# Kernel optimization log

Measured on AMD Instinct MI355X. Metric: run time of the kernel, lower is better.

Reference implementation:

```python
import jax, jax.numpy as jnp
import numpy as np

N, L, H, D = 4, 2048, 16, 32   # batch, seq len, heads, projection_dim
DIM = H * D                     # 512 model dim


def setup_inputs() -> dict:
    rng = jax.random.key(0)
    k1, k2, k3, k4, k5 = jax.random.split(rng, 5)
    query = jax.random.normal(k1, (N, L, DIM), dtype=jnp.float32)
    key = jax.random.normal(k2, (N, L, DIM), dtype=jnp.float32)
    scale = 0.02
    Wq = jax.random.normal(k3, (DIM, DIM), dtype=jnp.float32) * scale
    Wk = jax.random.normal(k4, (DIM, DIM), dtype=jnp.float32) * scale
    Wv = jax.random.normal(k5, (DIM, DIM), dtype=jnp.float32) * scale
    return {"query": query, "key": key, "Wq": Wq, "Wk": Wk, "Wv": Wv, "mask": 1}


def reference(query, key, Wq, Wk, Wv, mask):
    # torch Linear(bias=False): y = x @ W^T
    n, Lq, _ = query.shape
    _, Lk, _ = key.shape
    q = (query @ Wq.T).reshape(n, Lq, H, D).transpose(0, 2, 1, 3)  # (N,H,Lq,D)
    k = (key @ Wk.T).reshape(n, Lk, H, D).transpose(0, 2, 1, 3)    # (N,H,Lk,D)
    v = (key @ Wv.T).reshape(n, Lk, H, D).transpose(0, 2, 1, 3)    # (N,H,Lk,D)
    q = jax.nn.softmax(q, axis=-1)
    k = jax.nn.softmax(k, axis=-1)
    # causal branch (mask truthy): Lq*Lk > D^2*Lk, so the module takes the
    # cumsum-of-outer-products ("right") path:
    #   right = cumsum_l( k_l outer v_l );  out_l = q_l @ right_l
    kv = jnp.einsum('nhld,nhle->nhlde', k, v)   # (N,H,Lk,D,D) outer products
    S = jnp.cumsum(kv, axis=2)                  # running prefix state
    out = jnp.einsum('nhld,nhlde->nhle', q, S)  # (N,H,Lq,D)
    return out.transpose(0, 2, 1, 3).reshape(n, Lq, H * D)
```

## Files before the change

### kernel.cpp

```cpp
#include <hip/hip_runtime.h>

#define NB      4
#define L_SEQ   2048
#define H_HEADS 16
#define D32     32
#define DIM     512
#define NH      (NB * H_HEADS)
#define CHUNK   64
#define NCHUNK  (L_SEQ / CHUNK)

typedef __attribute__((ext_vector_type(8))) short bf16x8;
typedef __attribute__((ext_vector_type(4))) float f32x4;

__device__ __forceinline__ unsigned short f2bf(float x) {
    unsigned u = __float_as_uint(x);
    u += 0x7fff + ((u >> 16) & 1);
    return (unsigned short)(u >> 16);
}
__device__ __forceinline__ unsigned pack2(float lo, float hi) {
    return (unsigned)f2bf(lo) | ((unsigned)f2bf(hi) << 16);
}

#define QN  4194304
#define WN  262144
#define TOT (2*QN + 3*WN)
__global__ __launch_bounds__(256) void convert_kernel(
    const float* __restrict__ query, const float* __restrict__ key,
    const float* __restrict__ Wq, const float* __restrict__ Wk,
    const float* __restrict__ Wv, unsigned short* __restrict__ dst)
{
    int idx = (blockIdx.x * 256 + threadIdx.x) * 8;
    const float* src; int off;
    if (idx < QN)               { src = query; off = idx; }
    else if (idx < 2*QN)        { src = key;   off = idx - QN; }
    else if (idx < 2*QN + WN)   { src = Wq;    off = idx - 2*QN; }
    else if (idx < 2*QN + 2*WN) { src = Wk;    off = idx - 2*QN - WN; }
    else                        { src = Wv;    off = idx - 2*QN - 2*WN; }
    float4 a = *(const float4*)(src + off);
    float4 b = *(const float4*)(src + off + 4);
    *(uint4*)(dst + idx) = make_uint4(pack2(a.x, a.y), pack2(a.z, a.w),
                                      pack2(b.x, b.y), pack2(b.z, b.w));
}

__device__ __forceinline__ void softmax_heads(f32x4 (&acc)[4][4]) {
    #pragma unroll
    for (int i = 0; i < 4; i++)
        #pragma unroll
        for (int jp = 0; jp < 2; jp++)
            #pragma unroll
            for (int r = 0; r < 4; r++) {
                float a = acc[i][2 * jp][r], b = acc[i][2 * jp + 1][r];
                float m = fmaxf(a, b);
                #pragma unroll
                for (int off = 1; off < 16; off <<= 1)
                    m = fmaxf(m, __shfl_xor(m, off, 64));
                float ea = __expf(a - m), eb = __expf(b - m);
                float s = ea + eb;
                #pragma unroll
                for (int off = 1; off < 16; off <<= 1)
                    s += __shfl_xor(s, off, 64);
                float inv = 1.0f / s;
                acc[i][2 * jp][r]     = ea * inv;
                acc[i][2 * jp + 1][r] = eb * inv;
            }
}

__device__ __forceinline__ void scatter_qk(
    const f32x4 (&acc)[4][4], unsigned short* __restrict__ dp,
    int m0, int n0, int wm, int wn, int quad, int lm)
{
    #pragma unroll
    for (int i = 0; i < 4; i++) {
        int rbase = m0 + wm * 64 + i * 16 + quad * 4;
        #pragma unroll
        for (int r = 0; r < 4; r++) {
            int rg = rbase + r;
            int n = rg >> 11, l = rg & 2047;
            #pragma unroll
            for (int j = 0; j < 4; j++) {
                int cg = n0 + wn * 64 + j * 16 + lm;
                int h = cg >> 5, e = cg & 31;
                dp[(((size_t)(n * H_HEADS + h)) * L_SEQ + l) * D32 + e] =
                    f2bf(acc[i][j][r]);
            }
        }
    }
}

#define GLL(g, l) __builtin_amdgcn_global_load_lds( \
    (const __attribute__((address_space(1))) unsigned int*)(g), \
    (__attribute__((address_space(3))) unsigned int*)(l), 16, 0, 0)

__global__ __launch_bounds__(256, 2) void gemm3_mfma_kernel(
    const unsigned short* __restrict__ qb, const unsigned short* __restrict__ kb2,
    const unsigned short* __restrict__ wqb, const unsigned short* __restrict__ wkb,
    const unsigned short* __restrict__ wvb,
    unsigned short* __restrict__ Qs, unsigned short* __restrict__ Ks,
    unsigned short* __restrict__ Vt)
{
    const int z  = blockIdx.z;
    const int bx = blockIdx.x >> 6;
    const int by = blockIdx.x & 63;
    const int m0 = by * 128, n0 = bx * 128;

    const unsigned short* PA  = z ? kb2 : qb;
    const unsigned short* PB1 = z ? wkb : wqb;

    __shared__ unsigned short Asm[3 * 4096];
    __shared__ unsigned short B1sm[3 * 4096];
    __shared__ unsigned short B2sm[3 * 4096];

    const int t    = threadIdx.x;
    const int w    = t >> 6;
    const int lane = t & 63;
    const int wm   = w >> 1, wn = w & 1;
    const int lm   = lane & 15, quad = lane >> 4;

    const int qswz = quad ^ ((lm >> 1) & 3);
    const int aoff = (wm * 64 + lm) * 32 + qswz * 8;
    const int boff = (wn * 64 + lm) * 32 + qswz * 8;

    const int li0 = t, li1 = t + 256;
    const int row0 = li0 >> 2, row1 = li1 >> 2;
    const int qs0 = (li0 & 3) ^ ((li0 >> 3) & 3);
    const int qs1 = (li1 & 3) ^ ((li1 >> 3) & 3);
    const unsigned short* gA0 = PA  + (size_t)(m0 + row0) * DIM + qs0 * 8;
    const unsigned short* gA1 = PA  + (size_t)(m0 + row1) * DIM + qs1 * 8;
    const unsigned short* gB10 = PB1 + (size_t)(n0 + row0) * DIM + qs0 * 8;
    const unsigned short* gB11 = PB1 + (size_t)(n0 + row1) * DIM + qs1 * 8;

    if (z == 0) {
        f32x4 acc[4][4] = {};
#define STG0(buf, kb) do { \
        GLL(gA0  + (kb), Asm  + (buf) * 4096 + li0 * 8); \
        GLL(gB10 + (kb), B1sm + (buf) * 4096 + li0 * 8); \
        GLL(gA1  + (kb), Asm  + (buf) * 4096 + li1 * 8); \
        GLL(gB11 + (kb), B1sm + (buf) * 4096 + li1 * 8); \
} while (0)
        STG0(0, 0);
        STG0(1, 32);
        __builtin_amdgcn_sched_barrier(0);
        asm volatile("s_waitcnt vmcnt(4)" ::: "memory");
        __builtin_amdgcn_s_barrier();
        __builtin_amdgcn_sched_barrier(0);

        #pragma unroll
        for (int step = 0; step < 16; ++step) {
            const int cur = step % 3;
            if (step < 14) STG0((step + 2) % 3, (step + 2) * 32);
            const unsigned short* As = Asm + cur * 4096;
            const unsigned short* Bs = B1sm + cur * 4096;
            bf16x8 af[4], bf1[4];
            #pragma unroll
            for (int i = 0; i < 4; i++)
                af[i] = *(const bf16x8*)(As + aoff + i * 512);
            #pragma unroll
            for (int j = 0; j < 4; j++)
                bf1[j] = *(const bf16x8*)(Bs + boff + j * 512);
            #pragma unroll
            for (int i = 0; i < 4; i++)
                #pragma unroll
                for (int j = 0; j < 4; j++)
                    acc[i][j] = __builtin_amdgcn_mfma_f32_16x16x32_bf16(
                        af[i], bf1[j], acc[i][j], 0, 0, 0);
            __builtin_amdgcn_sched_barrier(0);
            if (step < 14)       asm volatile("s_waitcnt vmcnt(4)" ::: "memory");
            else if (step == 14) asm volatile("s_waitcnt vmcnt(0)" ::: "memory");
            if (step < 15) {
                __builtin_amdgcn_s_barrier();
                __builtin_amdgcn_sched_barrier(0);
            }
        }
#undef STG0
        softmax_heads(acc);
        scatter_qk(acc, Qs, m0, n0, wm, wn, quad, lm);
    } else {
        const unsigned short* gB20 = wvb + (size_t)(n0 + row0) * DIM + qs0 * 8;
        const unsigned short* gB21 = wvb + (size_t)(n0 + row1) * DIM + qs1 * 8;
        f32x4 acc[4][4] = {};
        f32x4 acc2[4][4] = {};
#define STG1(buf, kb) do { \
        GLL(gA0  + (kb), Asm  + (buf) * 4096 + li0 * 8); \
        GLL(gB10 + (kb), B1sm + (buf) * 4096 + li0 * 8); \
        GLL(gB20 + (kb), B2sm + (buf) * 4096 + li0 * 8); \
        GLL(gA1  + (kb), Asm  + (buf) * 4096 + li1 * 8); \
        GLL(gB11 + (kb), B1sm + (buf) * 4096 + li1 * 8); \
        GLL(gB21 + (kb), B2sm + (buf) * 4096 + li1 * 8); \
} while (0)
        STG1(0, 0);
        STG1(1, 32);
        __builtin_amdgcn_sched_barrier(0);
        asm volatile("s_waitcnt vmcnt(6)" ::: "memory");
        __builtin_amdgcn_s_barrier();
        __builtin_amdgcn_sched_barrier(0);

        #pragma unroll
        for (int step = 0; step < 16; ++step) {
            const int cur = step % 3;
            if (step < 14) STG1((step + 2) % 3, (step + 2) * 32);
            const unsigned short* As  = Asm  + cur * 4096;
            const unsigned short* B1s = B1sm + cur * 4096;
            const unsigned short* B2s = B2sm + cur * 4096;
            bf16x8 af[4], bf1[4], bf2[4];
            #pragma unroll
            for (int i = 0; i < 4; i++)
                af[i] = *(const bf16x8*)(As + aoff + i * 512);
            #pragma unroll
            for (int j = 0; j < 4; j++) {
                bf1[j] = *(const bf16x8*)(B1s + boff + j * 512);
                bf2[j] = *(const bf16x8*)(B2s + boff + j * 512);
            }
            #pragma unroll
            for (int i = 0; i < 4; i++)
                #pragma unroll
                for (int j = 0; j < 4; j++) {
                    acc[i][j]  = __builtin_amdgcn_mfma_f32_16x16x32_bf16(
                        af[i], bf1[j], acc[i][j], 0, 0, 0);
                    acc2[i][j] = __builtin_amdgcn_mfma_f32_16x16x32_bf16(
                        af[i], bf2[j], acc2[i][j], 0, 0, 0);
                }
            __builtin_amdgcn_sched_barrier(0);
            if (step < 14)       asm volatile("s_waitcnt vmcnt(6)" ::: "memory");
            else if (step == 14) asm volatile("s_waitcnt vmcnt(0)" ::: "memory");
            if (step < 15) {
                __builtin_amdgcn_s_barrier();
                __builtin_amdgcn_sched_barrier(0);
            }
        }
#undef STG1
        softmax_heads(acc);
        scatter_qk(acc, Ks, m0, n0, wm, wn, quad, lm);
        #pragma unroll
        for (int i = 0; i < 4; i++) {
            int lg0 = m0 + wm * 64 + i * 16 + quad * 4;
            int nb = lg0 >> 11, ll = lg0 & 2047;
            #pragma unroll
            for (int j = 0; j < 4; j++) {
                int cg = n0 + wn * 64 + j * 16 + lm;
                int h = cg >> 5, e = cg & 31;
                ushort4 u;
                u.x = f2bf(acc2[i][j][0]); u.y = f2bf(acc2[i][j][1]);
                u.z = f2bf(acc2[i][j][2]); u.w = f2bf(acc2[i][j][3]);
                *(ushort4*)(Vt + (((size_t)(nb * H_HEADS + h)) * D32 + e) * L_SEQ + ll) = u;
            }
        }
    }
}

__global__ __launch_bounds__(64) void chunk_kv_mfma_kernel(
    const unsigned short* __restrict__ Ks, const unsigned short* __restrict__ Vt,
    float* __restrict__ ckvT)
{
    const int c = blockIdx.x, nh = blockIdx.y;
    const int lane = threadIdx.x;
    const int lm = lane & 15, quad = lane >> 4;

    __shared__ unsigned short Kl[64 * 36];

    {
        const unsigned short* kg = Ks + ((size_t)nh * L_SEQ + c * CHUNK + lane) * D32;
        #pragma unroll
        for (int i = 0; i < 4; i++) {
            uint4 v = *(const uint4*)(kg + i * 8);
            *(uint4*)(Kl + lane * 36 + i * 8) = v;
        }
    }
    __syncthreads();

    f32x4 acc[2][2] = {};
    #pragma unroll
    for (int ch = 0; ch < 2; ch++) {
        bf16x8 aV[2], bK[2];
        #pragma unroll
        for (int mt = 0; mt < 2; mt++)
            aV[mt] = *(const bf16x8*)(Vt + ((size_t)nh * D32 + mt * 16 + lm) * L_SEQ
                                         + c * CHUNK + ch * 32 + quad * 8);
        #pragma unroll
        for (int nt = 0; nt < 2; nt++) {
            const unsigned short* kp = Kl + (ch * 32 + quad * 8) * 36 + nt * 16 + lm;
            #pragma unroll
            for (int j = 0; j < 8; j++) bK[nt][j] = (short)kp[j * 36];
        }
        #pragma unroll
        for (int mt = 0; mt < 2; mt++)
            #pragma unroll
            for (int nt = 0; nt < 2; nt++)
                acc[mt][nt] = __builtin_amdgcn_mfma_f32_16x16x32_bf16(
                    aV[mt], bK[nt], acc[mt][nt], 0, 0, 0);
    }
    #pragma unroll
    for (int mt = 0; mt < 2; mt++)
        #pragma unroll
        for (int nt = 0; nt < 2; nt++)
            #pragma unroll
            for (int r = 0; r < 4; r++) {
                int e = mt * 16 + quad * 4 + r;
                int d = nt * 16 + lm;
                ckvT[(((size_t)nh * NCHUNK + c) * 32 + e) * 32 + d] = acc[mt][nt][r];
            }
}

__global__ __launch_bounds__(64) void prefix_kernel(
    const float* __restrict__ ckvT, unsigned short* __restrict__ SpT)
{
    int nh   = blockIdx.y;
    int slot = blockIdx.x * 64 + threadIdx.x;
    const float* base = ckvT + (size_t)nh * NCHUNK * 1024 + slot * 4;
    unsigned short* sp = SpT + (size_t)nh * NCHUNK * 1024 + slot * 4;
    float4 acc = make_float4(0.f, 0.f, 0.f, 0.f);
    #pragma unroll
    for (int cb = 0; cb < NCHUNK; cb += 8) {
        float4 v[8];
        #pragma unroll
        for (int j = 0; j < 8; j++)
            v[j] = *(const float4*)(base + (size_t)(cb + j) * 1024);
        #pragma unroll
        for (int j = 0; j < 8; j++) {
            ushort4 u;
            u.x = f2bf(acc.x); u.y = f2bf(acc.y);
            u.z = f2bf(acc.z); u.w = f2bf(acc.w);
            *(ushort4*)(sp + (size_t)(cb + j) * 1024) = u;
            acc.x += v[j].x; acc.y += v[j].y;
            acc.z += v[j].z; acc.w += v[j].w;
        }
    }
}

__global__ __launch_bounds__(64) void chunk_out_mfma_kernel(
    const unsigned short* __restrict__ Qs, const unsigned short* __restrict__ Ks,
    const unsigned short* __restrict__ Vt, const unsigned short* __restrict__ SpT,
    float* __restrict__ out)
{
    const int c = blockIdx.x, nh = blockIdx.y;
    __shared__ unsigned short P[64 * 72];

    const int lane = threadIdx.x;
    const int lm = lane & 15, quad = lane >> 4;

    bf16x8 aQ[4], bK[4];
    #pragma unroll
    for (int i = 0; i < 4; i++)
        aQ[i] = *(const bf16x8*)(Qs + ((size_t)nh * L_SEQ + c * CHUNK + i * 16 + lm) * D32
                                    + quad * 8);
    #pragma unroll
    for (int j = 0; j < 4; j++)
        bK[j] = *(const bf16x8*)(Ks + ((size_t)nh * L_SEQ + c * CHUNK + j * 16 + lm) * D32
                                    + quad * 8);

    #pragma unroll
    for (int i = 0; i < 4; i++) {
        #pragma unroll
        for (int j = 0; j < 4; j++) {
            f32x4 p = {};
            if (j <= i) {
                p = __builtin_amdgcn_mfma_f32_16x16x32_bf16(aQ[i], bK[j], p, 0, 0, 0);
                if (j == i) {
                    #pragma unroll
                    for (int r = 0; r < 4; r++)
                        if (lm > quad * 4 + r) p[r] = 0.f;
                }
            }
            #pragma unroll
            for (int r = 0; r < 4; r++)
                P[(i * 16 + quad * 4 + r) * 72 + j * 16 + lm] = f2bf(p[r]);
        }
    }
    __syncthreads();

    bf16x8 bS[2], bV[2][2];
    #pragma unroll
    for (int nt = 0; nt < 2; nt++) {
        bS[nt] = *(const bf16x8*)(SpT + (((size_t)nh * NCHUNK + c) * 32 + nt * 16 + lm) * 32
                                      + quad * 8);
        #pragma unroll
        for (int ch = 0; ch < 2; ch++)
            bV[nt][ch] = *(const bf16x8*)(Vt + ((size_t)nh * D32 + nt * 16 + lm) * L_SEQ
                                             + c * CHUNK + ch * 32 + quad * 8);
    }

    const int n = nh >> 4, h = nh & 15;
    #pragma unroll
    for (int i = 0; i < 4; i++) {
        const int chmax = (i >> 1) + 1;
        bf16x8 aP[2];
        for (int ch = 0; ch < chmax; ch++)
            aP[ch] = *(const bf16x8*)&P[(i * 16 + lm) * 72 + ch * 32 + quad * 8];
        #pragma unroll
        for (int nt = 0; nt < 2; nt++) {
            f32x4 acc = {};
            acc = __builtin_amdgcn_mfma_f32_16x16x32_bf16(aQ[i], bS[nt], acc, 0, 0, 0);
            for (int ch = 0; ch < chmax; ch++)
                acc = __builtin_amdgcn_mfma_f32_16x16x32_bf16(aP[ch], bV[nt][ch], acc, 0, 0, 0);
            #pragma unroll
            for (int r = 0; r < 4; r++) {
                int lg = c * CHUNK + i * 16 + quad * 4 + r;
                out[((size_t)n * L_SEQ + lg) * DIM + h * D32 + nt * 16 + lm] = acc[r];
            }
        }
    }
}

extern "C" void kernel_launch(void* const* d_in, const int* in_sizes, int n_in,
                              void* d_out, int out_size, void* d_ws, size_t ws_size,
                              hipStream_t stream)
{
    (void)in_sizes; (void)n_in; (void)out_size; (void)ws_size;
    const float* query = (const float*)d_in[0];
    const float* key   = (const float*)d_in[1];
    const float* Wq    = (const float*)d_in[2];
    const float* Wk    = (const float*)d_in[3];
    const float* Wv    = (const float*)d_in[4];
    float* out = (float*)d_out;

    unsigned short* bf = (unsigned short*)d_ws;
    unsigned short* qb  = bf;
    unsigned short* kb  = qb + QN;
    unsigned short* wqb = kb + QN;
    unsigned short* wkb = wqb + WN;
    unsigned short* wvb = wkb + WN;
    unsigned short* Qs  = wvb + WN;
    const size_t SZ = (size_t)NH * L_SEQ * D32;
    unsigned short* Ks  = Qs + SZ;
    unsigned short* Vt  = Ks + SZ;
    unsigned short* SpT = Vt + SZ;
    float* ckvT = (float*)(SpT + (size_t)NH * NCHUNK * 1024);

    convert_kernel<<<dim3(TOT / (256 * 8)), dim3(256), 0, stream>>>(
        query, key, Wq, Wk, Wv, qb);
    gemm3_mfma_kernel<<<dim3(256, 1, 2), dim3(256), 0, stream>>>(
        qb, kb, wqb, wkb, wvb, Qs, Ks, Vt);
    chunk_kv_mfma_kernel<<<dim3(NCHUNK, NH), dim3(64), 0, stream>>>(Ks, Vt, ckvT);
    prefix_kernel<<<dim3(4, NH), dim3(64), 0, stream>>>(ckvT, SpT);
    chunk_out_mfma_kernel<<<dim3(NCHUNK, NH), dim3(64), 0, stream>>>(Qs, Ks, Vt, SpT, out);
}
```

Measured before the change: 133.6 us.

## Fuse chunk KV outer products and prefix scan into one per-head kernel

The GEMM epilogue now also writes a transposed K copy (KsT) next to V, so the chunk KV kernel can load K fragments directly instead of going through a strided LDS gather. Chunk KV products and the prefix scan are merged into a single kernel per (batch, head). Each block keeps all 32 chunk states in 128KB of LDS and scans them there, which removes the fp32 ckvT round trip through global memory and one launch. The cost is an extra global write of K, and only 64 blocks of 512 threads with heavy LDS use, so parallelism is much lower.

```diff
diff --git a/kernel.cpp b/kernel.cpp
--- a/kernel.cpp
+++ b/kernel.cpp
@@ -96,7 +96,7 @@
     const unsigned short* __restrict__ wqb, const unsigned short* __restrict__ wkb,
     const unsigned short* __restrict__ wvb,
     unsigned short* __restrict__ Qs, unsigned short* __restrict__ Ks,
-    unsigned short* __restrict__ Vt)
+    unsigned short* __restrict__ Vt, unsigned short* __restrict__ KsT)
 {
     const int z  = blockIdx.z;
     const int bx = blockIdx.x >> 6;
@@ -238,91 +238,71 @@
             for (int j = 0; j < 4; j++) {
                 int cg = n0 + wn * 64 + j * 16 + lm;
                 int h = cg >> 5, e = cg & 31;
-                ushort4 u;
-                u.x = f2bf(acc2[i][j][0]); u.y = f2bf(acc2[i][j][1]);
-                u.z = f2bf(acc2[i][j][2]); u.w = f2bf(acc2[i][j][3]);
-                *(ushort4*)(Vt + (((size_t)(nb * H_HEADS + h)) * D32 + e) * L_SEQ + ll) = u;
-            }
-        }
-    }
-}
-
-__global__ __launch_bounds__(64) void chunk_kv_mfma_kernel(
-    const unsigned short* __restrict__ Ks, const unsigned short* __restrict__ Vt,
-    float* __restrict__ ckvT)
-{
-    const int c = blockIdx.x, nh = blockIdx.y;
-    const int lane = threadIdx.x;
+                size_t base = (((size_t)(nb * H_HEADS + h)) * D32 + e) * L_SEQ + ll;
+                ushort4 uk, uv;
+                uk.x = f2bf(acc[i][j][0]);  uk.y = f2bf(acc[i][j][1]);
+                uk.z = f2bf(acc[i][j][2]);  uk.w = f2bf(acc[i][j][3]);
+                uv.x = f2bf(acc2[i][j][0]); uv.y = f2bf(acc2[i][j][1]);
+                uv.z = f2bf(acc2[i][j][2]); uv.w = f2bf(acc2[i][j][3]);
+                *(ushort4*)(KsT + base) = uk;
+                *(ushort4*)(Vt  + base) = uv;
+            }
+        }
+    }
+}
+
+__global__ __launch_bounds__(512) void kv_prefix_kernel(
+    const unsigned short* __restrict__ KsT, const unsigned short* __restrict__ Vt,
+    unsigned short* __restrict__ SpT)
+{
+    const int nh = blockIdx.x;
+    __shared__ float L[NCHUNK * 1024];
+
+    const int t = threadIdx.x;
+    const int w = t >> 6, lane = t & 63;
     const int lm = lane & 15, quad = lane >> 4;
 
-    __shared__ unsigned short Kl[64 * 36];
-
-    {
-        const unsigned short* kg = Ks + ((size_t)nh * L_SEQ + c * CHUNK + lane) * D32;
-        #pragma unroll
-        for (int i = 0; i < 4; i++) {
-            uint4 v = *(const uint4*)(kg + i * 8);
-            *(uint4*)(Kl + lane * 36 + i * 8) = v;
-        }
+    #pragma unroll
+    for (int cc = 0; cc < 4; cc++) {
+        const int c = w * 4 + cc;
+        f32x4 acc[2][2] = {};
+        #pragma unroll
+        for (int ch = 0; ch < 2; ch++) {
+            bf16x8 aV[2], bK[2];
+            #pragma unroll
+            for (int mt = 0; mt < 2; mt++)
+                aV[mt] = *(const bf16x8*)(Vt + ((size_t)nh * D32 + mt * 16 + lm) * L_SEQ
+                                             + c * CHUNK + ch * 32 + quad * 8);
+            #pragma unroll
+            for (int nt = 0; nt < 2; nt++)
+                bK[nt] = *(const bf16x8*)(KsT + ((size_t)nh * D32 + nt * 16 + lm) * L_SEQ
+                                              + c * CHUNK + ch * 32 + quad * 8);
+            #pragma unroll
+            for (int mt = 0; mt < 2; mt++)
+                #pragma unroll
+                for (int nt = 0; nt < 2; nt++)
+                    acc[mt][nt] = __builtin_amdgcn_mfma_f32_16x16x32_bf16(
+                        aV[mt], bK[nt], acc[mt][nt], 0, 0, 0);
+        }
+        #pragma unroll
+        for (int mt = 0; mt < 2; mt++)
+            #pragma unroll
+            for (int nt = 0; nt < 2; nt++)
+                #pragma unroll
+                for (int r = 0; r < 4; r++)
+                    L[c * 1024 + (mt * 16 + quad * 4 + r) * 32 + nt * 16 + lm]
+                        = acc[mt][nt][r];
     }
     __syncthreads();
 
-    f32x4 acc[2][2] = {};
-    #pragma unroll
-    for (int ch = 0; ch < 2; ch++) {
-        bf16x8 aV[2], bK[2];
-        #pragma unroll
-        for (int mt = 0; mt < 2; mt++)
-            aV[mt] = *(const bf16x8*)(Vt + ((size_t)nh * D32 + mt * 16 + lm) * L_SEQ
-                                         + c * CHUNK + ch * 32 + quad * 8);
-        #pragma unroll
-        for (int nt = 0; nt < 2; nt++) {
-            const unsigned short* kp = Kl + (ch * 32 + quad * 8) * 36 + nt * 16 + lm;
-            #pragma unroll
-            for (int j = 0; j < 8; j++) bK[nt][j] = (short)kp[j * 36];
-        }
-        #pragma unroll
-        for (int mt = 0; mt < 2; mt++)
-            #pragma unroll
-            for (int nt = 0; nt < 2; nt++)
-                acc[mt][nt] = __builtin_amdgcn_mfma_f32_16x16x32_bf16(
-                    aV[mt], bK[nt], acc[mt][nt], 0, 0, 0);
-    }
-    #pragma unroll
-    for (int mt = 0; mt < 2; mt++)
-        #pragma unroll
-        for (int nt = 0; nt < 2; nt++)
-            #pragma unroll
-            for (int r = 0; r < 4; r++) {
-                int e = mt * 16 + quad * 4 + r;
-                int d = nt * 16 + lm;
-                ckvT[(((size_t)nh * NCHUNK + c) * 32 + e) * 32 + d] = acc[mt][nt][r];
-            }
-}
-
-__global__ __launch_bounds__(64) void prefix_kernel(
-    const float* __restrict__ ckvT, unsigned short* __restrict__ SpT)
-{
-    int nh   = blockIdx.y;
-    int slot = blockIdx.x * 64 + threadIdx.x;
-    const float* base = ckvT + (size_t)nh * NCHUNK * 1024 + slot * 4;
-    unsigned short* sp = SpT + (size_t)nh * NCHUNK * 1024 + slot * 4;
-    float4 acc = make_float4(0.f, 0.f, 0.f, 0.f);
-    #pragma unroll
-    for (int cb = 0; cb < NCHUNK; cb += 8) {
-        float4 v[8];
-        #pragma unroll
-        for (int j = 0; j < 8; j++)
-            v[j] = *(const float4*)(base + (size_t)(cb + j) * 1024);
-        #pragma unroll
-        for (int j = 0; j < 8; j++) {
-            ushort4 u;
-            u.x = f2bf(acc.x); u.y = f2bf(acc.y);
-            u.z = f2bf(acc.z); u.w = f2bf(acc.w);
-            *(ushort4*)(sp + (size_t)(cb + j) * 1024) = u;
-            acc.x += v[j].x; acc.y += v[j].y;
-            acc.z += v[j].z; acc.w += v[j].w;
-        }
+    const int slot = t * 2;
+    float a0 = 0.f, a1 = 0.f;
+    unsigned short* sp = SpT + (size_t)nh * NCHUNK * 1024 + slot;
+    #pragma unroll
+    for (int c = 0; c < NCHUNK; c++) {
+        float2 v = *(const float2*)&L[c * 1024 + slot];
+        *(unsigned*)(sp + (size_t)c * 1024) = pack2(a0, a1);
+        a0 += v.x; a1 += v.y;
     }
 }
 
@@ -422,14 +402,14 @@
     const size_t SZ = (size_t)NH * L_SEQ * D32;
     unsigned short* Ks  = Qs + SZ;
     unsigned short* Vt  = Ks + SZ;
-    unsigned short* SpT = Vt + SZ;
-    float* ckvT = (float*)(SpT + (size_t)NH * NCHUNK * 1024);
+    unsigned short* KsT = Vt + SZ;
+    unsigned short* SpT = KsT + SZ;
 
     convert_kernel<<<dim3(TOT / (256 * 8)), dim3(256), 0, stream>>>(
         query, key, Wq, Wk, Wv, qb);
     gemm3_mfma_kernel<<<dim3(256, 1, 2), dim3(256), 0, stream>>>(
-        qb, kb, wqb, wkb, wvb, Qs, Ks, Vt);
-    chunk_kv_mfma_kernel<<<dim3(NCHUNK, NH), dim3(64), 0, stream>>>(Ks, Vt, ckvT);
-    prefix_kernel<<<dim3(4, NH), dim3(64), 0, stream>>>(ckvT, SpT);
-    chunk_out_mfma_kernel<<<dim3(NCHUNK, NH), dim3(64), 0, stream>>>(Qs, Ks, Vt, SpT, out);
-}
+        qb, kb, wqb, wkb, wvb, Qs, Ks, Vt, KsT);
+    kv_prefix_kernel<<<dim3(NH), dim3(512), 0, stream>>>(KsT, Vt, SpT);
+    chunk_out_mfma_kernel<<<dim3(NCHUNK, NH), dim3(64), 0, stream>>>(
+        Qs, Ks, Vt, SpT, out);
+}
```

Measured after the change: 135.2 us. About the same (+1.2%).
